# Optimization experiments

Measured on AMD Instinct MI355X. Metric: run time of the kernel, lower is better.

## Reference

```python
import jax, jax.numpy as jnp
import numpy as np

VOCAB = 40000
U = 128  # num_trans_units


def setup_inputs() -> dict:
    key = jax.random.key(0)
    ks = jax.random.split(key, 10)
    B, S, T, L = 16, 512, 64, 64
    sents = jax.random.randint(ks[0], (B, S), 0, 30000)
    triples = jax.random.randint(ks[1], (B, T, L, 3), 0, VOCAB)
    sent_triples = jax.random.randint(ks[2], (B, S, 1), 0, T)
    scale = 0.05
    emb_table = jax.random.normal(ks[3], (VOCAB, U), jnp.float32)
    W_trans = jax.random.normal(ks[4], (U, U), jnp.float32) * scale
    b_trans = jnp.zeros((U,), jnp.float32)
    W_ht = jax.random.normal(ks[5], (2 * U, U), jnp.float32) * scale
    b_ht = jnp.zeros((U,), jnp.float32)
    W_rel = jax.random.normal(ks[6], (U, U), jnp.float32) * scale
    b_rel = jnp.zeros((U,), jnp.float32)
    return {
        "sents": sents, "triples": triples, "sent_triples": sent_triples,
        "emb_table": emb_table,
        "W_trans": W_trans, "b_trans": b_trans,
        "W_ht": W_ht, "b_ht": b_ht,
        "W_rel": W_rel, "b_rel": b_rel,
    }


def reference(sents, triples, sent_triples, emb_table,
              W_trans, b_trans, W_ht, b_ht, W_rel, b_rel):
    # triples: [B, T, L, 3] int ids -> embed [B, T, L, 3, U]
    emb = emb_table[triples]
    # fc_trans_transform: Linear(U,U) + Tanh on last dim
    te = jnp.tanh(emb @ W_trans + b_trans)            # [B,T,L,3,U]
    head, relation, tail = te[..., 0, :], te[..., 1, :], te[..., 2, :]
    head_tail = jnp.concatenate([head, tail], axis=-1)  # [B,T,L,2U]
    ht_t = jnp.tanh(head_tail @ W_ht + b_ht)             # [B,T,L,U]
    rel_t = relation @ W_rel + b_rel                     # [B,T,L,U]
    e_weight = jnp.sum(rel_t * ht_t, axis=-1)            # [B,T,L]
    alpha = jax.nn.softmax(e_weight, axis=-1)            # over triple_len L
    graph_embed = jnp.sum(alpha[..., None] * head_tail, axis=2)  # [B,T,2U]
    # gather_nd: out[b, s] = graph_embed[b, sent_triples[b, s, 0]]
    idx = sent_triples[..., 0]                           # [B,S]
    out = jnp.take_along_axis(graph_embed, idx[:, :, None], axis=1)  # [B,S,2U]
    return out
```

## Files before the change

kernel.cpp:

```cpp
#include <hip/hip_runtime.h>
#include <cstdint>
#include <cstddef>

typedef short short8 __attribute__((ext_vector_type(8)));
typedef float f32x4 __attribute__((ext_vector_type(4)));

#define BB 16
#define SS 512
#define TT 64
#define LL 64
#define UU 128
#define NV 40000

#define WT_OFF    0u
#define WHT_OFF   (WT_OFF + 32768u)
#define WREL_OFF  (WHT_OFF + 65536u)
#define TE_OFF    (WREL_OFF + 32768u)

__device__ __forceinline__ unsigned short f2bf(float x) {
  unsigned u = __float_as_uint(x);
  unsigned r = ((u >> 16) & 1u) + 0x7FFFu;
  return (unsigned short)((u + r) >> 16);
}
__device__ __forceinline__ float ftanh(float x) {
  float e = __expf(2.0f * x);
  return 1.0f - __fdividef(2.0f, e + 1.0f);
}
__device__ __forceinline__ unsigned cvtpk(float a, float b) {
  unsigned r;
  asm("v_cvt_pk_bf16_f32 %0, %1, %2" : "=v"(r) : "v"(a), "v"(b));
  return r;
}
template<int CTRL>
__device__ __forceinline__ float dpp_mov(float x) {
  return __int_as_float(__builtin_amdgcn_update_dpp(
      0, __float_as_int(x), CTRL, 0xF, 0xF, true));
}
__device__ __forceinline__ float row16_sum(float x) {
  x += dpp_mov<0xB1>(x);
  x += dpp_mov<0x4E>(x);
  x += dpp_mov<0x141>(x);
  x += dpp_mov<0x140>(x);
  return x;
}
__device__ __forceinline__ float full64_sum(float x) {
  x = row16_sum(x);
  x += __shfl_xor(x, 16, 64);
  x += __shfl_xor(x, 32, 64);
  return x;
}
__device__ __forceinline__ float full64_max(float x) {
  x = fmaxf(x, dpp_mov<0xB1>(x));
  x = fmaxf(x, dpp_mov<0x4E>(x));
  x = fmaxf(x, dpp_mov<0x141>(x));
  x = fmaxf(x, dpp_mov<0x140>(x));
  x = fmaxf(x, __shfl_xor(x, 16, 64));
  x = fmaxf(x, __shfl_xor(x, 32, 64));
  return x;
}

__global__ void prep_kernel(const float* __restrict__ Wt,
                            const float* __restrict__ Wht,
                            const float* __restrict__ Wrel,
                            unsigned char* __restrict__ ws) {
  int slot = blockIdx.x * 256 + threadIdx.x;
  const float* W;
  unsigned char* base;
  if (slot < 2048)      { W = Wt;   base = ws + WT_OFF; }
  else if (slot < 6144) { W = Wht;  base = ws + WHT_OFF;  slot -= 2048; }
  else                  { W = Wrel; base = ws + WREL_OFF; slot -= 6144; }
  int lane = slot & 63, pair = slot >> 6;
  int n  = (pair & 7) * 16 + (lane & 15);
  int k0 = (pair >> 3) * 32 + (lane >> 4) * 8;
  short8 hv;
  #pragma unroll
  for (int j = 0; j < 8; ++j)
    hv[j] = (short)f2bf(W[(size_t)(k0 + j) * UU + n]);
  *reinterpret_cast<short8*>(base + (size_t)pair * 1024 + lane * 16) = hv;
}

__launch_bounds__(1024, 8)
__global__ void prep_te(const float* __restrict__ emb_f32,
                        const float* __restrict__ b_trans,
                        const unsigned char* __restrict__ wsr,
                        unsigned short* __restrict__ te_g) {
  __shared__ unsigned short TEB[192 * 128];
  const int tid  = threadIdx.x;
  const int base = blockIdx.x * 192;
  const int w    = tid >> 6;
  const int lane = tid & 63;
  const int li   = lane & 15;
  const int lg   = lane >> 4;
  const int nt   = w & 7;
  const int rh   = w >> 3;

  float4 xv[3], yv[3];
  #pragma unroll
  for (int j = 0; j < 3; ++j) {
    int o = tid + j * 1024, row = o >> 4, pc = o & 15;
    int grow = base + row; if (grow > NV - 1) grow = NV - 1;
    int clog = pc ^ (row & 15);
    const float* fb = emb_f32 + (size_t)grow * UU + clog * 8;
    xv[j] = *reinterpret_cast<const float4*>(fb);
    yv[j] = *reinterpret_cast<const float4*>(fb + 4);
  }
  const unsigned char* wtb = wsr + WT_OFF;
  short8 B1h[4];
  #pragma unroll
  for (int kt = 0; kt < 4; ++kt)
    B1h[kt] = *reinterpret_cast<const short8*>(
        wtb + (size_t)(kt * 8 + nt) * 1024 + lane * 16);
  #pragma unroll
  for (int j = 0; j < 3; ++j) {
    int o = tid + j * 1024;
    uint4 pk = { cvtpk(xv[j].x, xv[j].y), cvtpk(xv[j].z, xv[j].w),
                 cvtpk(yv[j].x, yv[j].y), cvtpk(yv[j].z, yv[j].w) };
    *reinterpret_cast<uint4*>(&TEB[o * 8]) = pk;
  }
  const float4 btr4 = *reinterpret_cast<const float4*>(b_trans + nt * 16 + lg * 4);
  __syncthreads();

  f32x4 acc[6];
  #pragma unroll
  for (int q = 0; q < 6; ++q) acc[q] = f32x4{0.f, 0.f, 0.f, 0.f};
  #pragma unroll
  for (int kt = 0; kt < 4; ++kt) {
    #pragma unroll
    for (int q = 0; q < 6; ++q) {
      const short8 b = *reinterpret_cast<const short8*>(
          &TEB[((rh * 6 + q) * 16 + li) * 128 + (((kt * 4 + lg) ^ li) << 3)]);
      acc[q] = __builtin_amdgcn_mfma_f32_16x16x32_bf16(B1h[kt], b, acc[q], 0, 0, 0);
    }
  }

  #pragma unroll
  for (int q = 0; q < 6; ++q) {
    int row  = (rh * 6 + q) * 16 + li;
    int grow = base + row; if (grow > NV - 1) grow = NV - 1;
    float v0 = ftanh(acc[q][0] + btr4.x);
    float v1 = ftanh(acc[q][1] + btr4.y);
    float v2 = ftanh(acc[q][2] + btr4.z);
    float v3 = ftanh(acc[q][3] + btr4.w);
    uint2 pk = { cvtpk(v0, v1), cvtpk(v2, v3) };
    *reinterpret_cast<uint2*>(te_g + (size_t)grow * UU + nt * 16 + lg * 4) = pk;
  }
}

__launch_bounds__(1024, 8)
__global__ void fused_bt(const int* __restrict__ triples,
                         const unsigned short* __restrict__ te_g,
                         const float* __restrict__ b_ht,
                         const float* __restrict__ b_rel,
                         const int* __restrict__ sent_triples,
                         const unsigned char* __restrict__ wsr,
                         float* __restrict__ out) {
  __shared__ unsigned short TEB[192 * 128];
  __shared__ float EWt[8][64];
  __shared__ float PART[8][256];
  __shared__ int MATCH[512];
  __shared__ int NM;

  const int tid  = threadIdx.x;
  const int bt   = blockIdx.x;
  const int w    = tid >> 6;
  const int lane = tid & 63;
  const int li   = lane & 15;
  const int lg   = lane >> 4;
  const int nt   = w & 7;
  const int rh   = w >> 3;

  int tok[3];
  #pragma unroll
  for (int j = 0; j < 3; ++j) {
    int row = (tid + j * 1024) >> 4;
    tok[j] = triples[(size_t)bt * 192 + row];
  }
  int sidx = -1;
  if (tid < SS) sidx = sent_triples[(size_t)(bt >> 6) * SS + tid];
  if (tid == 0) NM = 0;

  short8 sv[3];
  #pragma unroll
  for (int j = 0; j < 3; ++j) {
    int o = tid + j * 1024, row = o >> 4, pc = o & 15;
    int clog = pc ^ (row & 15);
    sv[j] = *reinterpret_cast<const short8*>(
        te_g + (size_t)tok[j] * UU + clog * 8);
  }
  #pragma unroll
  for (int j = 0; j < 3; ++j)
    *reinterpret_cast<short8*>(&TEB[(tid + j * 1024) * 8]) = sv[j];

  const unsigned char* whtb = wsr + WHT_OFF;
  const unsigned char* wrlb = wsr + WREL_OFF;
  const float bhv  = b_ht[nt * 16 + li];
  const float brlv = b_rel[nt * 16 + li];
  short8 Wc = *reinterpret_cast<const short8*>(
      whtb + (size_t)nt * 1024 + lane * 16);
  __syncthreads();

  if (sidx == (bt & 63))
    MATCH[atomicAdd(&NM, 1)] = tid;

  const int mh = rh * 2;
  f32x4 accH[2] = {{0.f,0.f,0.f,0.f},{0.f,0.f,0.f,0.f}};
  f32x4 accR[2] = {{0.f,0.f,0.f,0.f},{0.f,0.f,0.f,0.f}};

  #pragma unroll
  for (int kt = 0; kt < 8; ++kt) {
    short8 Wn;
    if (kt < 7)
      Wn = *reinterpret_cast<const short8*>(
          whtb + (size_t)((kt + 1) * 8 + nt) * 1024 + lane * 16);
    else
      Wn = *reinterpret_cast<const short8*>(
          wrlb + (size_t)nt * 1024 + lane * 16);
    const int koff = (kt < 4) ? 0 : 2;
    const int c16  = (kt & 3) * 4 + lg;
    #pragma unroll
    for (int mi = 0; mi < 2; ++mi) {
      const int row = 48 * (mh + mi) + 3 * li + koff;
      const short8 a = *reinterpret_cast<const short8*>(
          &TEB[row * 128 + ((c16 ^ (row & 15)) << 3)]);
      accH[mi] = __builtin_amdgcn_mfma_f32_16x16x32_bf16(a, Wc, accH[mi], 0, 0, 0);
    }
    Wc = Wn;
  }
  #pragma unroll
  for (int kt = 0; kt < 4; ++kt) {
    short8 Wn;
    if (kt < 3)
      Wn = *reinterpret_cast<const short8*>(
          wrlb + (size_t)((kt + 1) * 8 + nt) * 1024 + lane * 16);
    const int c16 = kt * 4 + lg;
    #pragma unroll
    for (int mi = 0; mi < 2; ++mi) {
      const int row = 48 * (mh + mi) + 3 * li + 1;
      const short8 a = *reinterpret_cast<const short8*>(
          &TEB[row * 128 + ((c16 ^ (row & 15)) << 3)]);
      accR[mi] = __builtin_amdgcn_mfma_f32_16x16x32_bf16(a, Wc, accR[mi], 0, 0, 0);
    }
    Wc = Wn;
  }

  #pragma unroll
  for (int mi = 0; mi < 2; ++mi) {
    #pragma unroll
    for (int r = 0; r < 4; ++r) {
      float p = ftanh(accH[mi][r] + bhv) * (accR[mi][r] + brlv);
      p = row16_sum(p);
      if (li == 0) EWt[nt][(mh + mi) * 16 + lg * 4 + r] = p;
    }
  }
  __syncthreads();

  float alpha;
  {
    float e = 0.f;
    #pragma unroll
    for (int n = 0; n < 8; ++n) e += EWt[n][lane];
    float mx = full64_max(e);
    float ex = __expf(e - mx);
    float sm = full64_sum(ex);
    alpha = ex / sm;
  }

  {
    int cp  = tid & 127, lgp = w >> 1;
    int c0  = cp << 1;
    int k   = (c0 >> 7) << 1;
    int cc  = c0 & 127;
    int w8  = cc >> 3, bofs = (cc & 7) << 1;
    float o0 = 0.f, o1 = 0.f;
    #pragma unroll
    for (int j = 0; j < 8; ++j) {
      int l = lgp * 8 + j;
      float al = __int_as_float(
          __builtin_amdgcn_readlane(__float_as_int(alpha), l));
      int row = 3 * l + k;
      unsigned u = *reinterpret_cast<const unsigned*>(
          reinterpret_cast<const char*>(TEB) + row * 256 +
          (((w8 ^ (row & 15)) << 4) | bofs));
      o0 = fmaf(al, __uint_as_float(u << 16), o0);
      o1 = fmaf(al, __uint_as_float(u & 0xFFFF0000u), o1);
    }
    *reinterpret_cast<float2*>(&PART[lgp][c0]) = make_float2(o0, o1);
  }
  __syncthreads();

  {
    const int b  = bt >> 6;
    const int nm = NM;
    if (w < nm) {
      float4 v = {0.f, 0.f, 0.f, 0.f};
      #pragma unroll
      for (int g = 0; g < 8; ++g) {
        float4 p = reinterpret_cast<const float4*>(&PART[g][0])[lane];
        v.x += p.x; v.y += p.y; v.z += p.z; v.w += p.w;
      }
      for (int q = w; q < nm; q += 16) {
        int s = MATCH[q];
        reinterpret_cast<float4*>(out + ((size_t)(b * SS + s)) * 256)[lane] = v;
      }
    }
  }
}

extern "C" void kernel_launch(void* const* d_in, const int* in_sizes, int n_in,
                              void* d_out, int out_size, void* d_ws, size_t ws_size,
                              hipStream_t stream) {
  const int*   triples      = (const int*)d_in[1];
  const int*   sent_triples = (const int*)d_in[2];
  const float* emb_table    = (const float*)d_in[3];
  const float* W_trans      = (const float*)d_in[4];
  const float* b_trans      = (const float*)d_in[5];
  const float* W_ht         = (const float*)d_in[6];
  const float* b_ht         = (const float*)d_in[7];
  const float* W_rel        = (const float*)d_in[8];
  const float* b_rel        = (const float*)d_in[9];
  float* out = (float*)d_out;
  unsigned char* ws = (unsigned char*)d_ws;
  unsigned short* te_g = (unsigned short*)(ws + TE_OFF);

  prep_kernel<<<32, 256, 0, stream>>>(W_trans, W_ht, W_rel, ws);
  prep_te<<<(NV + 191) / 192, 1024, 0, stream>>>(emb_table, b_trans, ws, te_g);
  fused_bt<<<BB * TT, 1024, 0, stream>>>(
      triples, te_g, b_ht, b_rel, sent_triples, ws, out);
}
```

Measured before the change: 43.36 us.

## Precompute relation projection per vocab row in prep kernel, gather it in fused kernel

The relation transform (te @ W_rel + b_rel) now runs once per vocabulary row inside the prep kernel and is written to a fp32 workspace table. The fused per-(b,t) kernel then gathers only the head/tail te rows into shared memory and reads the per-lane relation values directly from that table. This drops the relation MFMA loop and a third of the shared tile per block. In exchange the prep kernel does an extra GEMM over all 40000 rows and writes a 20MB fp32 table, and the main kernel does scattered fp32 gathers.

```diff
diff --git a/kernel.cpp b/kernel.cpp
--- a/kernel.cpp
+++ b/kernel.cpp
@@ -16,6 +16,7 @@
 #define WHT_OFF   (WT_OFF + 32768u)
 #define WREL_OFF  (WHT_OFF + 65536u)
 #define TE_OFF    (WREL_OFF + 32768u)
+#define R_OFF     (TE_OFF + 40000u*128u*2u)
 
 __device__ __forceinline__ unsigned short f2bf(float x) {
   unsigned u = __float_as_uint(x);
@@ -79,11 +80,13 @@
   *reinterpret_cast<short8*>(base + (size_t)pair * 1024 + lane * 16) = hv;
 }
 
-__launch_bounds__(1024, 8)
-__global__ void prep_te(const float* __restrict__ emb_f32,
-                        const float* __restrict__ b_trans,
-                        const unsigned char* __restrict__ wsr,
-                        unsigned short* __restrict__ te_g) {
+__launch_bounds__(1024, 4)
+__global__ void prep_teR(const float* __restrict__ emb_f32,
+                         const float* __restrict__ b_trans,
+                         const float* __restrict__ b_rel,
+                         const unsigned char* __restrict__ wsr,
+                         unsigned short* __restrict__ te_g,
+                         float* __restrict__ R_g) {
   __shared__ unsigned short TEB[192 * 128];
   const int tid  = threadIdx.x;
   const int base = blockIdx.x * 192;
@@ -104,7 +107,8 @@
     xv[j] = *reinterpret_cast<const float4*>(fb);
     yv[j] = *reinterpret_cast<const float4*>(fb + 4);
   }
-  const unsigned char* wtb = wsr + WT_OFF;
+  const unsigned char* wtb  = wsr + WT_OFF;
+  const unsigned char* wrlb = wsr + WREL_OFF;
   short8 B1h[4];
   #pragma unroll
   for (int kt = 0; kt < 4; ++kt)
@@ -132,7 +136,10 @@
       acc[q] = __builtin_amdgcn_mfma_f32_16x16x32_bf16(B1h[kt], b, acc[q], 0, 0, 0);
     }
   }
-
+  __syncthreads();
+
+  const int cc8 = nt * 2 + (lg >> 1);
+  const int hb8 = (lg & 1) << 3;
   #pragma unroll
   for (int q = 0; q < 6; ++q) {
     int row  = (rh * 6 + q) * 16 + li;
@@ -142,19 +149,46 @@
     float v2 = ftanh(acc[q][2] + btr4.z);
     float v3 = ftanh(acc[q][3] + btr4.w);
     uint2 pk = { cvtpk(v0, v1), cvtpk(v2, v3) };
+    *reinterpret_cast<uint2*>(
+        reinterpret_cast<char*>(TEB) + row * 256 + (((cc8 ^ li) << 4) | hb8)) = pk;
     *reinterpret_cast<uint2*>(te_g + (size_t)grow * UU + nt * 16 + lg * 4) = pk;
+  }
+  __syncthreads();
+
+  const float4 brl4 = *reinterpret_cast<const float4*>(b_rel + nt * 16 + lg * 4);
+  f32x4 a2[6];
+  #pragma unroll
+  for (int q = 0; q < 6; ++q) a2[q] = f32x4{0.f, 0.f, 0.f, 0.f};
+  #pragma unroll
+  for (int kt = 0; kt < 4; ++kt) {
+    const short8 Wf = *reinterpret_cast<const short8*>(
+        wrlb + (size_t)(kt * 8 + nt) * 1024 + lane * 16);
+    #pragma unroll
+    for (int q = 0; q < 6; ++q) {
+      const short8 b = *reinterpret_cast<const short8*>(
+          &TEB[((rh * 6 + q) * 16 + li) * 128 + (((kt * 4 + lg) ^ li) << 3)]);
+      a2[q] = __builtin_amdgcn_mfma_f32_16x16x32_bf16(Wf, b, a2[q], 0, 0, 0);
+    }
+  }
+  #pragma unroll
+  for (int q = 0; q < 6; ++q) {
+    int row  = (rh * 6 + q) * 16 + li;
+    int grow = base + row; if (grow > NV - 1) grow = NV - 1;
+    float4 v = { a2[q][0] + brl4.x, a2[q][1] + brl4.y,
+                 a2[q][2] + brl4.z, a2[q][3] + brl4.w };
+    *reinterpret_cast<float4*>(R_g + (size_t)grow * UU + nt * 16 + lg * 4) = v;
   }
 }
 
 __launch_bounds__(1024, 8)
 __global__ void fused_bt(const int* __restrict__ triples,
                          const unsigned short* __restrict__ te_g,
+                         const float* __restrict__ R_g,
                          const float* __restrict__ b_ht,
-                         const float* __restrict__ b_rel,
                          const int* __restrict__ sent_triples,
                          const unsigned char* __restrict__ wsr,
                          float* __restrict__ out) {
-  __shared__ unsigned short TEB[192 * 128];
+  __shared__ unsigned short TEB[128 * 128];
   __shared__ float EWt[8][64];
   __shared__ float PART[8][256];
   __shared__ int MATCH[512];
@@ -168,33 +202,47 @@
   const int lg   = lane >> 4;
   const int nt   = w & 7;
   const int rh   = w >> 3;
-
-  int tok[3];
-  #pragma unroll
-  for (int j = 0; j < 3; ++j) {
+  const int mh   = rh * 2;
+  const int* tb  = triples + (size_t)bt * 192;
+
+  int stok[2];
+  #pragma unroll
+  for (int j = 0; j < 2; ++j) {
     int row = (tid + j * 1024) >> 4;
-    tok[j] = triples[(size_t)bt * 192 + row];
-  }
+    stok[j] = tb[3 * (row & 63) + ((row >> 6) << 1)];
+  }
+  int rtok[2][4];
+  #pragma unroll
+  for (int mi = 0; mi < 2; ++mi)
+    #pragma unroll
+    for (int r = 0; r < 4; ++r)
+      rtok[mi][r] = tb[3 * ((mh + mi) * 16 + lg * 4 + r) + 1];
+
   int sidx = -1;
   if (tid < SS) sidx = sent_triples[(size_t)(bt >> 6) * SS + tid];
   if (tid == 0) NM = 0;
 
-  short8 sv[3];
-  #pragma unroll
-  for (int j = 0; j < 3; ++j) {
+  short8 sv[2];
+  #pragma unroll
+  for (int j = 0; j < 2; ++j) {
     int o = tid + j * 1024, row = o >> 4, pc = o & 15;
     int clog = pc ^ (row & 15);
     sv[j] = *reinterpret_cast<const short8*>(
-        te_g + (size_t)tok[j] * UU + clog * 8);
-  }
-  #pragma unroll
-  for (int j = 0; j < 3; ++j)
+        te_g + (size_t)stok[j] * UU + clog * 8);
+  }
+  float Rv[2][4];
+  #pragma unroll
+  for (int mi = 0; mi < 2; ++mi)
+    #pragma unroll
+    for (int r = 0; r < 4; ++r)
+      Rv[mi][r] = R_g[(size_t)rtok[mi][r] * UU + nt * 16 + li];
+
+  #pragma unroll
+  for (int j = 0; j < 2; ++j)
     *reinterpret_cast<short8*>(&TEB[(tid + j * 1024) * 8]) = sv[j];
 
   const unsigned char* whtb = wsr + WHT_OFF;
-  const unsigned char* wrlb = wsr + WREL_OFF;
-  const float bhv  = b_ht[nt * 16 + li];
-  const float brlv = b_rel[nt * 16 + li];
+  const float bhv = b_ht[nt * 16 + li];
   short8 Wc = *reinterpret_cast<const short8*>(
       whtb + (size_t)nt * 1024 + lane * 16);
   __syncthreads();
@@ -202,52 +250,30 @@
   if (sidx == (bt & 63))
     MATCH[atomicAdd(&NM, 1)] = tid;
 
-  const int mh = rh * 2;
   f32x4 accH[2] = {{0.f,0.f,0.f,0.f},{0.f,0.f,0.f,0.f}};
-  f32x4 accR[2] = {{0.f,0.f,0.f,0.f},{0.f,0.f,0.f,0.f}};
-
   #pragma unroll
   for (int kt = 0; kt < 8; ++kt) {
     short8 Wn;
     if (kt < 7)
       Wn = *reinterpret_cast<const short8*>(
           whtb + (size_t)((kt + 1) * 8 + nt) * 1024 + lane * 16);
-    else
-      Wn = *reinterpret_cast<const short8*>(
-          wrlb + (size_t)nt * 1024 + lane * 16);
-    const int koff = (kt < 4) ? 0 : 2;
-    const int c16  = (kt & 3) * 4 + lg;
+    const int hb  = (kt < 4) ? 0 : 64;
+    const int c16 = (kt & 3) * 4 + lg;
     #pragma unroll
     for (int mi = 0; mi < 2; ++mi) {
-      const int row = 48 * (mh + mi) + 3 * li + koff;
+      const int row = hb + (mh + mi) * 16 + li;
       const short8 a = *reinterpret_cast<const short8*>(
-          &TEB[row * 128 + ((c16 ^ (row & 15)) << 3)]);
+          &TEB[row * 128 + ((c16 ^ li) << 3)]);
       accH[mi] = __builtin_amdgcn_mfma_f32_16x16x32_bf16(a, Wc, accH[mi], 0, 0, 0);
     }
-    Wc = Wn;
-  }
-  #pragma unroll
-  for (int kt = 0; kt < 4; ++kt) {
-    short8 Wn;
-    if (kt < 3)
-      Wn = *reinterpret_cast<const short8*>(
-          wrlb + (size_t)((kt + 1) * 8 + nt) * 1024 + lane * 16);
-    const int c16 = kt * 4 + lg;
-    #pragma unroll
-    for (int mi = 0; mi < 2; ++mi) {
-      const int row = 48 * (mh + mi) + 3 * li + 1;
-      const short8 a = *reinterpret_cast<const short8*>(
-          &TEB[row * 128 + ((c16 ^ (row & 15)) << 3)]);
-      accR[mi] = __builtin_amdgcn_mfma_f32_16x16x32_bf16(a, Wc, accR[mi], 0, 0, 0);
-    }
-    Wc = Wn;
+    if (kt < 7) Wc = Wn;
   }
 
   #pragma unroll
   for (int mi = 0; mi < 2; ++mi) {
     #pragma unroll
     for (int r = 0; r < 4; ++r) {
-      float p = ftanh(accH[mi][r] + bhv) * (accR[mi][r] + brlv);
+      float p = ftanh(accH[mi][r] + bhv) * Rv[mi][r];
       p = row16_sum(p);
       if (li == 0) EWt[nt][(mh + mi) * 16 + lg * 4 + r] = p;
     }
@@ -268,16 +294,16 @@
   {
     int cp  = tid & 127, lgp = w >> 1;
     int c0  = cp << 1;
-    int k   = (c0 >> 7) << 1;
+    int k   = c0 >> 7;
     int cc  = c0 & 127;
     int w8  = cc >> 3, bofs = (cc & 7) << 1;
     float o0 = 0.f, o1 = 0.f;
     #pragma unroll
     for (int j = 0; j < 8; ++j) {
-      int l = lgp * 8 + j;
+      int lr  = lgp * 8 + j;
       float al = __int_as_float(
-          __builtin_amdgcn_readlane(__float_as_int(alpha), l));
-      int row = 3 * l + k;
+          __builtin_amdgcn_readlane(__float_as_int(alpha), lr));
+      int row = (k << 6) + lr;
       unsigned u = *reinterpret_cast<const unsigned*>(
           reinterpret_cast<const char*>(TEB) + row * 256 +
           (((w8 ^ (row & 15)) << 4) | bofs));
@@ -295,8 +321,8 @@
       float4 v = {0.f, 0.f, 0.f, 0.f};
       #pragma unroll
       for (int g = 0; g < 8; ++g) {
-        float4 p = reinterpret_cast<const float4*>(&PART[g][0])[lane];
-        v.x += p.x; v.y += p.y; v.z += p.z; v.w += p.w;
+        float4 pp = reinterpret_cast<const float4*>(&PART[g][0])[lane];
+        v.x += pp.x; v.y += pp.y; v.z += pp.z; v.w += pp.w;
       }
       for (int q = w; q < nm; q += 16) {
         int s = MATCH[q];
@@ -321,9 +347,11 @@
   float* out = (float*)d_out;
   unsigned char* ws = (unsigned char*)d_ws;
   unsigned short* te_g = (unsigned short*)(ws + TE_OFF);
+  float* R_g = (float*)(ws + R_OFF);
 
   prep_kernel<<<32, 256, 0, stream>>>(W_trans, W_ht, W_rel, ws);
-  prep_te<<<(NV + 191) / 192, 1024, 0, stream>>>(emb_table, b_trans, ws, te_g);
+  prep_teR<<<(NV + 191) / 192, 1024, 0, stream>>>(
+      emb_table, b_trans, b_rel, ws, te_g, R_g);
   fused_bt<<<BB * TT, 1024, 0, stream>>>(
-      triples, te_g, b_ht, b_rel, sent_triples, ws, out);
-}
+      triples, te_g, R_g, b_ht, sent_triples, ws, out);
+}
```

After: 47.50 us. 9.6% more time.

## Fold weight prep into prep_te and halve its block size

Applied to the files above, without the earlier changes.

Removes the separate prep_kernel launch. Each prep_te wave now converts its W_trans fragment from fp32 to bf16 in registers instead of reading a pre-swizzled workspace copy, and the first 12 blocks also write the W_ht and W_rel bf16 layouts that fused_bt reads. prep_te blocks shrink from 1024 to 512 threads covering 96 rows each, which doubles the block count. The intent is to drop one kernel launch and its dependency gap. The cost is redundant strided fp32 loads of W_trans in every block.

```diff
diff --git a/kernel.cpp b/kernel.cpp
--- a/kernel.cpp
+++ b/kernel.cpp
@@ -12,8 +12,7 @@
 #define UU 128
 #define NV 40000
 
-#define WT_OFF    0u
-#define WHT_OFF   (WT_OFF + 32768u)
+#define WHT_OFF   0u
 #define WREL_OFF  (WHT_OFF + 65536u)
 #define TE_OFF    (WREL_OFF + 32768u)
 
@@ -59,60 +58,43 @@
   return x;
 }
 
-__global__ void prep_kernel(const float* __restrict__ Wt,
-                            const float* __restrict__ Wht,
-                            const float* __restrict__ Wrel,
-                            unsigned char* __restrict__ ws) {
-  int slot = blockIdx.x * 256 + threadIdx.x;
-  const float* W;
-  unsigned char* base;
-  if (slot < 2048)      { W = Wt;   base = ws + WT_OFF; }
-  else if (slot < 6144) { W = Wht;  base = ws + WHT_OFF;  slot -= 2048; }
-  else                  { W = Wrel; base = ws + WREL_OFF; slot -= 6144; }
-  int lane = slot & 63, pair = slot >> 6;
-  int n  = (pair & 7) * 16 + (lane & 15);
-  int k0 = (pair >> 3) * 32 + (lane >> 4) * 8;
-  short8 hv;
-  #pragma unroll
-  for (int j = 0; j < 8; ++j)
-    hv[j] = (short)f2bf(W[(size_t)(k0 + j) * UU + n]);
-  *reinterpret_cast<short8*>(base + (size_t)pair * 1024 + lane * 16) = hv;
-}
-
-__launch_bounds__(1024, 8)
+__launch_bounds__(512, 8)
 __global__ void prep_te(const float* __restrict__ emb_f32,
+                        const float* __restrict__ Wt,
+                        const float* __restrict__ Wht,
+                        const float* __restrict__ Wrel,
                         const float* __restrict__ b_trans,
-                        const unsigned char* __restrict__ wsr,
+                        unsigned char* __restrict__ ws,
                         unsigned short* __restrict__ te_g) {
-  __shared__ unsigned short TEB[192 * 128];
+  __shared__ unsigned short TEB[96 * 128];
   const int tid  = threadIdx.x;
-  const int base = blockIdx.x * 192;
+  const int base = blockIdx.x * 96;
   const int w    = tid >> 6;
   const int lane = tid & 63;
   const int li   = lane & 15;
   const int lg   = lane >> 4;
-  const int nt   = w & 7;
-  const int rh   = w >> 3;
+  const int nt   = w;
 
   float4 xv[3], yv[3];
   #pragma unroll
   for (int j = 0; j < 3; ++j) {
-    int o = tid + j * 1024, row = o >> 4, pc = o & 15;
+    int o = tid + j * 512, row = o >> 4, pc = o & 15;
     int grow = base + row; if (grow > NV - 1) grow = NV - 1;
     int clog = pc ^ (row & 15);
     const float* fb = emb_f32 + (size_t)grow * UU + clog * 8;
     xv[j] = *reinterpret_cast<const float4*>(fb);
     yv[j] = *reinterpret_cast<const float4*>(fb + 4);
   }
-  const unsigned char* wtb = wsr + WT_OFF;
   short8 B1h[4];
   #pragma unroll
-  for (int kt = 0; kt < 4; ++kt)
-    B1h[kt] = *reinterpret_cast<const short8*>(
-        wtb + (size_t)(kt * 8 + nt) * 1024 + lane * 16);
+  for (int kt = 0; kt < 4; ++kt) {
+    #pragma unroll
+    for (int j = 0; j < 8; ++j)
+      B1h[kt][j] = (short)f2bf(Wt[(size_t)(kt * 32 + lg * 8 + j) * UU + nt * 16 + li]);
+  }
   #pragma unroll
   for (int j = 0; j < 3; ++j) {
-    int o = tid + j * 1024;
+    int o = tid + j * 512;
     uint4 pk = { cvtpk(xv[j].x, xv[j].y), cvtpk(xv[j].z, xv[j].w),
                  cvtpk(yv[j].x, yv[j].y), cvtpk(yv[j].z, yv[j].w) };
     *reinterpret_cast<uint4*>(&TEB[o * 8]) = pk;
@@ -128,14 +110,14 @@
     #pragma unroll
     for (int q = 0; q < 6; ++q) {
       const short8 b = *reinterpret_cast<const short8*>(
-          &TEB[((rh * 6 + q) * 16 + li) * 128 + (((kt * 4 + lg) ^ li) << 3)]);
+          &TEB[(q * 16 + li) * 128 + (((kt * 4 + lg) ^ li) << 3)]);
       acc[q] = __builtin_amdgcn_mfma_f32_16x16x32_bf16(B1h[kt], b, acc[q], 0, 0, 0);
     }
   }
 
   #pragma unroll
   for (int q = 0; q < 6; ++q) {
-    int row  = (rh * 6 + q) * 16 + li;
+    int row  = q * 16 + li;
     int grow = base + row; if (grow > NV - 1) grow = NV - 1;
     float v0 = ftanh(acc[q][0] + btr4.x);
     float v1 = ftanh(acc[q][1] + btr4.y);
@@ -143,6 +125,22 @@
     float v3 = ftanh(acc[q][3] + btr4.w);
     uint2 pk = { cvtpk(v0, v1), cvtpk(v2, v3) };
     *reinterpret_cast<uint2*>(te_g + (size_t)grow * UU + nt * 16 + lg * 4) = pk;
+  }
+
+  if (blockIdx.x < 12) {
+    int slot = blockIdx.x * 512 + tid;
+    const float* W;
+    unsigned char* fb;
+    if (slot < 4096) { W = Wht;  fb = ws + WHT_OFF; }
+    else             { W = Wrel; fb = ws + WREL_OFF; slot -= 4096; }
+    int ln = slot & 63, pair = slot >> 6;
+    int n  = (pair & 7) * 16 + (ln & 15);
+    int k0 = (pair >> 3) * 32 + (ln >> 4) * 8;
+    short8 hv;
+    #pragma unroll
+    for (int j = 0; j < 8; ++j)
+      hv[j] = (short)f2bf(W[(size_t)(k0 + j) * UU + n]);
+    *reinterpret_cast<short8*>(fb + (size_t)pair * 1024 + ln * 16) = hv;
   }
 }
 
@@ -322,8 +320,8 @@
   unsigned char* ws = (unsigned char*)d_ws;
   unsigned short* te_g = (unsigned short*)(ws + TE_OFF);
 
-  prep_kernel<<<32, 256, 0, stream>>>(W_trans, W_ht, W_rel, ws);
-  prep_te<<<(NV + 191) / 192, 1024, 0, stream>>>(emb_table, b_trans, ws, te_g);
+  prep_te<<<(NV + 95) / 96, 512, 0, stream>>>(
+      emb_table, W_trans, W_ht, W_rel, b_trans, ws, te_g);
   fused_bt<<<BB * TT, 1024, 0, stream>>>(
       triples, te_g, b_ht, b_rel, sent_triples, ws, out);
 }
```

Result: faster. 40.48 us, median of 2 (-6.6%).
